# Kernel optimization log

Hardware: AMD Instinct MI355X
Metric: run time of the kernel (lower is better)

The kernel has to match this reference:

```python
import jax, jax.numpy as jnp
import numpy as np

NUM_CLASSES = 512


def setup_inputs() -> dict:
    key = jax.random.key(0)
    k1, k2 = jax.random.split(key)
    support_data = jax.random.normal(k1, (2560, 64, 5, 5), dtype=jnp.float32)
    query_data = jax.random.normal(k2, (8192, 64, 5, 5), dtype=jnp.float32)
    # every class 0..511 appears exactly 5 times (sorted, like unique() ordering)
    support_label = (jnp.arange(2560, dtype=jnp.int32) // 5).astype(jnp.int32)
    return {"support_data": support_data, "query_data": query_data,
            "support_label": support_label}


def reference(support_data, query_data, support_label):
    # embedding_net == identity: embeddings are the raw (N, C, H, W) tensors.
    n_q = query_data.shape[0]
    d = support_data.shape[1] * support_data.shape[2] * support_data.shape[3]
    s = support_data.reshape(support_data.shape[0], d)   # [Ns, d]
    q = query_data.reshape(n_q, d)                        # [Nq, d]

    # class-mean prototypes (scatter-mean == per-unique-label mean loop)
    sums = jax.ops.segment_sum(s, support_label, num_segments=NUM_CLASSES)      # [M, d]
    counts = jax.ops.segment_sum(jnp.ones((s.shape[0],), s.dtype),
                                 support_label, num_segments=NUM_CLASSES)       # [M]
    protos = sums / counts[:, None]                                             # [M, d]

    # squared euclidean distance: ||q||^2 + ||p||^2 - 2 q.p  (same math as
    # broadcast (q - p)**2 summed over c,h,w, without the [Nq,M,d] intermediate)
    q2 = jnp.sum(q * q, axis=1, keepdims=True)            # [Nq, 1]
    p2 = jnp.sum(protos * protos, axis=1)                 # [M]
    dist = q2 + p2[None, :] - 2.0 * (q @ protos.T)        # [Nq, M]

    return jax.nn.log_softmax(-dist, axis=1)
```

## Files before the change

kernel.cpp:

```cpp
#include <hip/hip_runtime.h>
#include <hip/hip_bf16.h>
#include <cstdint>
#include <cstddef>

#define NS 2560
#define NQ 8192
#define NC 512
#define DD 1600

typedef __bf16 bf16_t;
typedef __bf16 bf16x4 __attribute__((ext_vector_type(4)));
typedef __bf16 bf16x8 __attribute__((ext_vector_type(8)));
typedef float f32x4 __attribute__((ext_vector_type(4)));

__global__ __launch_bounds__(256) void proto_kernel(
    const float* __restrict__ sup, const int* __restrict__ lab,
    bf16_t* __restrict__ protos, float* __restrict__ p2)
{
    const int m   = blockIdx.x;
    const int tid = threadIdx.x;
    __shared__ int   idxs[32];
    __shared__ int   cnt;
    __shared__ float wsum[4];
    if (tid == 0) cnt = 0;
    __syncthreads();
    for (int i = tid; i < NS; i += 256) {
        if (lab[i] == m) {
            int p = atomicAdd(&cnt, 1);
            if (p < 32) idxs[p] = i;
        }
    }
    __syncthreads();
    int n = cnt < 32 ? cnt : 32;
    if (tid == 0 && n > 1) {
        for (int a = 1; a < n; ++a) {
            int key = idxs[a]; int b = a - 1;
            while (b >= 0 && idxs[b] > key) { idxs[b+1] = idxs[b]; --b; }
            idxs[b+1] = key;
        }
    }
    __syncthreads();

    float acc[7];
    #pragma unroll
    for (int u = 0; u < 7; ++u) acc[u] = 0.f;
    for (int t = 0; t < n; ++t) {
        const float* src = sup + (size_t)idxs[t] * DD;
        #pragma unroll
        for (int u = 0; u < 7; ++u) {
            int j = tid + u * 256;
            if (j < DD) acc[u] += src[j];
        }
    }
    float inv = (n > 0) ? 1.f / (float)n : 0.f;
    float psq = 0.f;
    #pragma unroll
    for (int u = 0; u < 7; ++u) {
        int j = tid + u * 256;
        if (j < DD) {
            float p = acc[u] * inv;
            bf16_t pb = (bf16_t)p;
            protos[(size_t)m * DD + j] = pb;
            float pf = (float)pb;
            psq += pf * pf;
        }
    }
    #pragma unroll
    for (int o = 32; o > 0; o >>= 1) psq += __shfl_xor(psq, o);
    int lane = tid & 63, wid = tid >> 6;
    if (lane == 0) wsum[wid] = psq;
    __syncthreads();
    if (tid == 0) p2[m] = wsum[0] + wsum[1] + wsum[2] + wsum[3];
}

__device__ __forceinline__ void stage_B(const bf16_t* __restrict__ pb,
                                        char* bbuf, int k0, int tid, int wid)
{
    #pragma unroll
    for (int p = 0; p < 8; ++p) {
        int idx  = p * 256 + tid;
        int row  = idx >> 3;
        int gcol = (idx & 7) ^ (row & 7);
        const bf16_t* src = pb + (size_t)row * DD + k0 + gcol * 8;
        char* dst = bbuf + (size_t)(p * 256 + wid * 64) * 16;
        __builtin_amdgcn_global_load_lds(
            (const __attribute__((address_space(1))) void*)src,
            (__attribute__((address_space(3))) void*)dst, 16, 0, 0);
    }
}

__global__ __launch_bounds__(256, 2) void gemm_kernel(
    const float* __restrict__ q, const bf16_t* __restrict__ protos,
    const float* __restrict__ p2, float* __restrict__ out)
{
    extern __shared__ char smem[];

    const int tid  = threadIdx.x;
    const int lane = tid & 63;
    const int wid  = tid >> 6;
    const int r    = lane & 15;
    const int g    = lane >> 4;
    const int m0   = blockIdx.x * 32;
    const int n0   = blockIdx.y * 256;

    const bf16_t* pb = protos + (size_t)n0 * DD;

    float p2c[4];
    #pragma unroll
    for (int ni = 0; ni < 4; ++ni) p2c[ni] = p2[n0 + wid * 64 + ni * 16 + r];

    f32x4 acc[2][4];
    #pragma unroll
    for (int mi = 0; mi < 2; ++mi)
        #pragma unroll
        for (int ni = 0; ni < 4; ++ni)
            acc[mi][ni] = (f32x4){0.f, 0.f, 0.f, 0.f};

    const int ar0 = tid >> 4, ac0 = tid & 15;
    const int ar1 = (256 + tid) >> 4, ac1 = tid & 15;
    const float* ap0 = q + (size_t)(m0 + ar0) * DD + ac0 * 4;
    const float* ap1 = q + (size_t)(m0 + ar1) * DD + ac1 * 4;
    const int ao0 = (ar0 * 128 + ac0 * 8) ^ ((ar0 & 7) << 4);
    const int ao1 = (ar1 * 128 + ac1 * 8) ^ ((ar1 & 7) << 4);

    {
        float4 f0 = *(const float4*)(ap0);
        float4 f1 = *(const float4*)(ap1);
        stage_B(pb, smem, 0, tid, wid);
        bf16x4 w0, w1;
        w0[0] = (bf16_t)f0.x; w0[1] = (bf16_t)f0.y; w0[2] = (bf16_t)f0.z; w0[3] = (bf16_t)f0.w;
        w1[0] = (bf16_t)f1.x; w1[1] = (bf16_t)f1.y; w1[2] = (bf16_t)f1.z; w1[3] = (bf16_t)f1.w;
        *(bf16x4*)(smem + 65536 + ao0) = w0;
        *(bf16x4*)(smem + 65536 + ao1) = w1;
        __syncthreads();
    }

    for (int t = 0; t < 25; ++t) {
        const int cur = t & 1;
        const char* bs  = smem + cur * 32768;
        char*       bsn = smem + (cur ^ 1) * 32768;
        const char* as  = smem + 65536 + cur * 4096;
        char*       asn = smem + 65536 + (cur ^ 1) * 4096;
        const bool  pre = (t < 24);

        float4 fA0, fA1;
        if (pre) {
            fA0 = *(const float4*)(ap0 + (t + 1) * 64);
            fA1 = *(const float4*)(ap1 + (t + 1) * 64);
            stage_B(pb, bsn, (t + 1) * 64, tid, wid);
        }

        #pragma unroll
        for (int kk = 0; kk < 2; ++kk) {
            bf16x8 af[2], bfr[4];
            #pragma unroll
            for (int mi = 0; mi < 2; ++mi) {
                int ab = ((mi * 16 + r) * 128 + kk * 64 + g * 16) ^ ((r & 7) << 4);
                af[mi] = *(const bf16x8*)(as + ab);
            }
            #pragma unroll
            for (int ni = 0; ni < 4; ++ni) {
                int c  = wid * 64 + ni * 16 + r;
                int bb = (c * 128 + kk * 64 + g * 16) ^ ((c & 7) << 4);
                bfr[ni] = *(const bf16x8*)(bs + bb);
            }
            #pragma unroll
            for (int mi = 0; mi < 2; ++mi)
                #pragma unroll
                for (int ni = 0; ni < 4; ++ni)
                    acc[mi][ni] = __builtin_amdgcn_mfma_f32_16x16x32_bf16(
                        af[mi], bfr[ni], acc[mi][ni], 0, 0, 0);
        }

        if (pre) {
            bf16x4 w0, w1;
            w0[0] = (bf16_t)fA0.x; w0[1] = (bf16_t)fA0.y;
            w0[2] = (bf16_t)fA0.z; w0[3] = (bf16_t)fA0.w;
            w1[0] = (bf16_t)fA1.x; w1[1] = (bf16_t)fA1.y;
            w1[2] = (bf16_t)fA1.z; w1[3] = (bf16_t)fA1.w;
            *(bf16x4*)(asn + ao0) = w0;
            *(bf16x4*)(asn + ao1) = w1;
        }
        __syncthreads();
    }

    #pragma unroll
    for (int mi = 0; mi < 2; ++mi) {
        #pragma unroll
        for (int j = 0; j < 4; ++j) {
            size_t rowoff = (size_t)(m0 + mi * 16 + g * 4 + j) * NC + n0;
            #pragma unroll
            for (int ni = 0; ni < 4; ++ni)
                out[rowoff + wid * 64 + ni * 16 + r] =
                    2.f * acc[mi][ni][j] - p2c[ni];
        }
    }
}

__global__ __launch_bounds__(256) void lsm_kernel(float* __restrict__ io)
{
    const int row  = blockIdx.x * 4 + (threadIdx.x >> 6);
    const int lane = threadIdx.x & 63;
    float* p = io + (size_t)row * NC + lane * 8;

    float4 a = *(const float4*)(p);
    float4 b = *(const float4*)(p + 4);
    float v[8] = {a.x, a.y, a.z, a.w, b.x, b.y, b.z, b.w};

    float mx = v[0];
    #pragma unroll
    for (int i = 1; i < 8; ++i) mx = fmaxf(mx, v[i]);
    #pragma unroll
    for (int o = 32; o > 0; o >>= 1) mx = fmaxf(mx, __shfl_xor(mx, o));
    float se = 0.f;
    #pragma unroll
    for (int i = 0; i < 8; ++i) se += expf(v[i] - mx);
    #pragma unroll
    for (int o = 32; o > 0; o >>= 1) se += __shfl_xor(se, o);
    float lz = mx + logf(se);

    float4 o1 = {v[0]-lz, v[1]-lz, v[2]-lz, v[3]-lz};
    float4 o2 = {v[4]-lz, v[5]-lz, v[6]-lz, v[7]-lz};
    *(float4*)(p)     = o1;
    *(float4*)(p + 4) = o2;
}

extern "C" void kernel_launch(void* const* d_in, const int* in_sizes, int n_in,
                              void* d_out, int out_size, void* d_ws, size_t ws_size,
                              hipStream_t stream)
{
    const float* sup = (const float*)d_in[0];
    const float* qry = (const float*)d_in[1];
    const int*   lab = (const int*)d_in[2];
    float* out = (float*)d_out;

    char* ws = (char*)d_ws;
    bf16_t* protos = (bf16_t*)ws;
    float*  p2     = (float*)(ws + 1638400);

    const int smem_bytes = 73728;
    hipFuncSetAttribute(reinterpret_cast<const void*>(gemm_kernel),
                        hipFuncAttributeMaxDynamicSharedMemorySize, smem_bytes);

    proto_kernel<<<NC, 256, 0, stream>>>(sup, lab, protos, p2);
    gemm_kernel<<<dim3(NQ / 32, 2), 256, smem_bytes, stream>>>(qry, protos, p2, out);
    lsm_kernel<<<NQ / 4, 256, 0, stream>>>(out);
}
```

Measured before the change: 56.17 us.

## Drop double buffering in GEMM to fit four blocks per CU

Replaces the double-buffered LDS pipeline with a single buffer of 36 KB, so each K-step loads and then computes with two barriers. The launch bound rises to 4 blocks per CU and dynamic shared memory is replaced by static. This gives up overlap of global loads with MFMA work inside a block, relying instead on more resident blocks to hide latency. It also removes the hipFuncSetAttribute host call.

```diff
diff --git a/kernel.cpp b/kernel.cpp
--- a/kernel.cpp
+++ b/kernel.cpp
@@ -89,11 +89,11 @@
     }
 }
 
-__global__ __launch_bounds__(256, 2) void gemm_kernel(
+__global__ __launch_bounds__(256, 4) void gemm_kernel(
     const float* __restrict__ q, const bf16_t* __restrict__ protos,
     const float* __restrict__ p2, float* __restrict__ out)
 {
-    extern __shared__ char smem[];
+    __shared__ char smem[36864];
 
     const int tid  = threadIdx.x;
     const int lane = tid & 63;
@@ -123,32 +123,21 @@
     const int ao0 = (ar0 * 128 + ac0 * 8) ^ ((ar0 & 7) << 4);
     const int ao1 = (ar1 * 128 + ac1 * 8) ^ ((ar1 & 7) << 4);
 
-    {
-        float4 f0 = *(const float4*)(ap0);
-        float4 f1 = *(const float4*)(ap1);
-        stage_B(pb, smem, 0, tid, wid);
+    char* Bs = smem;
+    char* As = smem + 32768;
+
+    for (int t = 0; t < 25; ++t) {
+        float4 f0 = *(const float4*)(ap0 + t * 64);
+        float4 f1 = *(const float4*)(ap1 + t * 64);
+        stage_B(pb, Bs, t * 64, tid, wid);
         bf16x4 w0, w1;
-        w0[0] = (bf16_t)f0.x; w0[1] = (bf16_t)f0.y; w0[2] = (bf16_t)f0.z; w0[3] = (bf16_t)f0.w;
-        w1[0] = (bf16_t)f1.x; w1[1] = (bf16_t)f1.y; w1[2] = (bf16_t)f1.z; w1[3] = (bf16_t)f1.w;
-        *(bf16x4*)(smem + 65536 + ao0) = w0;
-        *(bf16x4*)(smem + 65536 + ao1) = w1;
+        w0[0] = (bf16_t)f0.x; w0[1] = (bf16_t)f0.y;
+        w0[2] = (bf16_t)f0.z; w0[3] = (bf16_t)f0.w;
+        w1[0] = (bf16_t)f1.x; w1[1] = (bf16_t)f1.y;
+        w1[2] = (bf16_t)f1.z; w1[3] = (bf16_t)f1.w;
+        *(bf16x4*)(As + ao0) = w0;
+        *(bf16x4*)(As + ao1) = w1;
         __syncthreads();
-    }
-
-    for (int t = 0; t < 25; ++t) {
-        const int cur = t & 1;
-        const char* bs  = smem + cur * 32768;
-        char*       bsn = smem + (cur ^ 1) * 32768;
-        const char* as  = smem + 65536 + cur * 4096;
-        char*       asn = smem + 65536 + (cur ^ 1) * 4096;
-        const bool  pre = (t < 24);
-
-        float4 fA0, fA1;
-        if (pre) {
-            fA0 = *(const float4*)(ap0 + (t + 1) * 64);
-            fA1 = *(const float4*)(ap1 + (t + 1) * 64);
-            stage_B(pb, bsn, (t + 1) * 64, tid, wid);
-        }
 
         #pragma unroll
         for (int kk = 0; kk < 2; ++kk) {
@@ -156,13 +145,13 @@
             #pragma unroll
             for (int mi = 0; mi < 2; ++mi) {
                 int ab = ((mi * 16 + r) * 128 + kk * 64 + g * 16) ^ ((r & 7) << 4);
-                af[mi] = *(const bf16x8*)(as + ab);
+                af[mi] = *(const bf16x8*)(As + ab);
             }
             #pragma unroll
             for (int ni = 0; ni < 4; ++ni) {
                 int c  = wid * 64 + ni * 16 + r;
                 int bb = (c * 128 + kk * 64 + g * 16) ^ ((c & 7) << 4);
-                bfr[ni] = *(const bf16x8*)(bs + bb);
+                bfr[ni] = *(const bf16x8*)(Bs + bb);
             }
             #pragma unroll
             for (int mi = 0; mi < 2; ++mi)
@@ -171,16 +160,6 @@
                     acc[mi][ni] = __builtin_amdgcn_mfma_f32_16x16x32_bf16(
                         af[mi], bfr[ni], acc[mi][ni], 0, 0, 0);
         }
-
-        if (pre) {
-            bf16x4 w0, w1;
-            w0[0] = (bf16_t)fA0.x; w0[1] = (bf16_t)fA0.y;
-            w0[2] = (bf16_t)fA0.z; w0[3] = (bf16_t)fA0.w;
-            w1[0] = (bf16_t)fA1.x; w1[1] = (bf16_t)fA1.y;
-            w1[2] = (bf16_t)fA1.z; w1[3] = (bf16_t)fA1.w;
-            *(bf16x4*)(asn + ao0) = w0;
-            *(bf16x4*)(asn + ao1) = w1;
-        }
         __syncthreads();
     }
 
@@ -238,11 +217,7 @@
     bf16_t* protos = (bf16_t*)ws;
     float*  p2     = (float*)(ws + 1638400);
 
-    const int smem_bytes = 73728;
-    hipFuncSetAttribute(reinterpret_cast<const void*>(gemm_kernel),
-                        hipFuncAttributeMaxDynamicSharedMemorySize, smem_bytes);
-
     proto_kernel<<<NC, 256, 0, stream>>>(sup, lab, protos, p2);
-    gemm_kernel<<<dim3(NQ / 32, 2), 256, smem_bytes, stream>>>(qry, protos, p2, out);
+    gemm_kernel<<<dim3(NQ / 32, 2), 256, 0, stream>>>(qry, protos, p2, out);
     lsm_kernel<<<NQ / 4, 256, 0, stream>>>(out);
 }
```

Result: no change. 57.08 us (+1.6%).
